# Optimization experiments

Measured on AMD Instinct MI355X. Metric: run time of the kernel, lower is better.

## Reference

```python
import jax, jax.numpy as jnp
import numpy as np

B, S, H, NH, L, V = 1, 2048, 2048, 16, 2, 32000
HD = H // NH            # 128 head dim
ROT = int(HD * 0.25)    # 32 rotary dims
BASE = 10000.0
EPS = 1e-5


def gelu(x):
    # GPT-NeoX tanh-approx gelu (matches the @torch.jit.script gelu)
    val = 0.79788456 * x * (1.0 + 0.044715 * x * x)
    return x * 0.5 * (1.0 + jnp.tanh(val))


def layernorm(x, g, b):
    m = jnp.mean(x, axis=-1, keepdims=True)
    v = jnp.var(x, axis=-1, keepdims=True)
    return (x - m) / jnp.sqrt(v + EPS) * g + b


def rope_cos_sin(seq_len):
    inv_freq = 1.0 / (BASE ** (jnp.arange(0, ROT, 2, dtype=jnp.float32) / ROT))
    t = jnp.arange(seq_len, dtype=jnp.float32)
    freqs = jnp.outer(t, inv_freq)             # [S, ROT/2]
    emb = jnp.concatenate([freqs, freqs], -1)  # [S, ROT]
    return jnp.cos(emb), jnp.sin(emb)


def rotate_half(x):
    half = x.shape[-1] // 2
    return jnp.concatenate([-x[..., half:], x[..., :half]], axis=-1)


def setup_inputs():
    key = jax.random.key(0)
    ks = jax.random.split(key, 8)
    s = 0.02
    return {
        "tokens": jax.random.randint(ks[0], (B, S), 0, V, dtype=jnp.int32),
        "embed": jax.random.normal(ks[1], (V, H), jnp.float32) * s,
        "ln1_g": jnp.ones((L, H), jnp.float32), "ln1_b": jnp.zeros((L, H), jnp.float32),
        "ln2_g": jnp.ones((L, H), jnp.float32), "ln2_b": jnp.zeros((L, H), jnp.float32),
        "qkv_w": jax.random.normal(ks[2], (L, 3 * H, H), jnp.float32) * s,
        "qkv_b": jnp.zeros((L, 3 * H), jnp.float32),
        "attn_out_w": jax.random.normal(ks[3], (L, H, H), jnp.float32) * s,
        "attn_out_b": jnp.zeros((L, H), jnp.float32),
        "fc1_w": jax.random.normal(ks[4], (L, 4 * H, H), jnp.float32) * s,
        "fc1_b": jnp.zeros((L, 4 * H), jnp.float32),
        "fc2_w": jax.random.normal(ks[5], (L, H, 4 * H), jnp.float32) * s,
        "fc2_b": jnp.zeros((L, H), jnp.float32),
        "lnf_g": jnp.ones((H,), jnp.float32), "lnf_b": jnp.zeros((H,), jnp.float32),
        "logits_w": jax.random.normal(ks[6], (V, H), jnp.float32) * s,
    }


def _attn_block(x, qw, qb, ow, ob, cos, sin, mask):
    b, s, _ = x.shape
    qkv = (x @ qw.T + qb).reshape(b, s, NH, 3 * HD)
    q, k, v = qkv[..., :HD], qkv[..., HD:2 * HD], qkv[..., 2 * HD:]
    c = cos[None, :, None, :]
    sn = sin[None, :, None, :]
    q = jnp.concatenate([q[..., :ROT] * c + rotate_half(q[..., :ROT]) * sn, q[..., ROT:]], -1)
    k = jnp.concatenate([k[..., :ROT] * c + rotate_half(k[..., :ROT]) * sn, k[..., ROT:]], -1)
    scores = jnp.einsum('bqhd,bkhd->bhqk', q, k) / jnp.float32(np.sqrt(HD))
    scores = jnp.where(mask, scores, jnp.float32(-10000.0))  # masked_fill -10000
    probs = jax.nn.softmax(scores, axis=-1)
    ctx = jnp.einsum('bhqk,bkhd->bqhd', probs, v).reshape(b, s, H)
    return ctx @ ow.T + ob


def reference(tokens, embed, ln1_g, ln1_b, ln2_g, ln2_b, qkv_w, qkv_b,
              attn_out_w, attn_out_b, fc1_w, fc1_b, fc2_w, fc2_b,
              lnf_g, lnf_b, logits_w):
    seq = tokens.shape[1]
    mask = jnp.tril(jnp.ones((1, 1, seq, seq), dtype=bool))
    cos, sin = rope_cos_sin(seq)
    h = embed[tokens]  # [B,S,H]
    for i in range(L):
        attn = _attn_block(layernorm(h, ln1_g[i], ln1_b[i]),
                           qkv_w[i], qkv_b[i], attn_out_w[i], attn_out_b[i],
                           cos, sin, mask)
        mlp_in = layernorm(h, ln2_g[i], ln2_b[i])
        mlp = gelu(mlp_in @ fc1_w[i].T + fc1_b[i]) @ fc2_w[i].T + fc2_b[i]
        h = h + mlp + attn  # parallel residual
    h = layernorm(h, lnf_g, lnf_b)
    logits = h @ logits_w.T
    return logits
```

## Files before the change

### kernel.cpp

```cpp
#include <hip/hip_runtime.h>
#include <cstdint>
#include <cstddef>

#define S_ 2048
#define H_ 2048
#define NH_ 16
#define HD_ 128
#define L_ 2
#define V_ 32000
#define ROT_ 32

typedef __bf16 bf16x8 __attribute__((ext_vector_type(8)));
typedef float f32x4 __attribute__((ext_vector_type(4)));

__device__ __forceinline__ unsigned short f2bf(float f) {
    unsigned u = __builtin_bit_cast(unsigned, f);
    unsigned r = u + 0x7fffu + ((u >> 16) & 1u);
    return (unsigned short)(r >> 16);
}
__device__ __forceinline__ float bf2f(unsigned short h) {
    return __builtin_bit_cast(float, (unsigned)h << 16);
}
__device__ __forceinline__ float gelu_f(float x) {
    float t = 0.79788456f * x * (1.0f + 0.044715f * x * x);
    return x * 0.5f * (1.0f + tanhf(t));
}

__global__ __launch_bounds__(256) void k_embed(const int* __restrict__ tok,
                                               const float* __restrict__ emb,
                                               float* __restrict__ h) {
    int s = blockIdx.x;
    int t = tok[s];
    const float4* src = (const float4*)(emb + (size_t)t * H_);
    float4* dst = (float4*)(h + (size_t)s * H_);
    for (int i = threadIdx.x; i < H_ / 4; i += 256) dst[i] = src[i];
}

__global__ __launch_bounds__(256) void k_ln(const float* __restrict__ x,
                                            const float* __restrict__ g,
                                            const float* __restrict__ b,
                                            unsigned short* __restrict__ out) {
    int s = blockIdx.x;
    int tid = threadIdx.x;
    const float4* xr = (const float4*)(x + (size_t)s * H_);
    float4 v0 = xr[tid], v1 = xr[tid + 256];
    float s1 = v0.x + v0.y + v0.z + v0.w + v1.x + v1.y + v1.z + v1.w;
    float s2 = v0.x * v0.x + v0.y * v0.y + v0.z * v0.z + v0.w * v0.w +
               v1.x * v1.x + v1.y * v1.y + v1.z * v1.z + v1.w * v1.w;
    #pragma unroll
    for (int off = 32; off > 0; off >>= 1) {
        s1 += __shfl_down(s1, off);
        s2 += __shfl_down(s2, off);
    }
    __shared__ float red[2][4];
    int wave = tid >> 6, lane = tid & 63;
    if (lane == 0) { red[0][wave] = s1; red[1][wave] = s2; }
    __syncthreads();
    s1 = red[0][0] + red[0][1] + red[0][2] + red[0][3];
    s2 = red[1][0] + red[1][1] + red[1][2] + red[1][3];
    float mean = s1 * (1.0f / H_);
    float var = s2 * (1.0f / H_) - mean * mean;
    float rstd = rsqrtf(var + 1e-5f);
    unsigned short* orow = out + (size_t)s * H_;
    int e0 = tid * 4, e1 = (tid + 256) * 4;
    unsigned short h0 = f2bf((v0.x - mean) * rstd * g[e0 + 0] + b[e0 + 0]);
    unsigned short h1 = f2bf((v0.y - mean) * rstd * g[e0 + 1] + b[e0 + 1]);
    unsigned short h2 = f2bf((v0.z - mean) * rstd * g[e0 + 2] + b[e0 + 2]);
    unsigned short h3 = f2bf((v0.w - mean) * rstd * g[e0 + 3] + b[e0 + 3]);
    uint2 p0; p0.x = h0 | ((unsigned)h1 << 16); p0.y = h2 | ((unsigned)h3 << 16);
    ((uint2*)orow)[tid] = p0;
    h0 = f2bf((v1.x - mean) * rstd * g[e1 + 0] + b[e1 + 0]);
    h1 = f2bf((v1.y - mean) * rstd * g[e1 + 1] + b[e1 + 1]);
    h2 = f2bf((v1.z - mean) * rstd * g[e1 + 2] + b[e1 + 2]);
    h3 = f2bf((v1.w - mean) * rstd * g[e1 + 3] + b[e1 + 3]);
    uint2 p1; p1.x = h0 | ((unsigned)h1 << 16); p1.y = h2 | ((unsigned)h3 << 16);
    ((uint2*)orow)[tid + 256] = p1;
}

template <bool BF16OUT, bool GELU, bool BIAS>
__global__ __launch_bounds__(256) void k_gemm(const unsigned short* __restrict__ A,
                                              const float* __restrict__ W,
                                              const float* __restrict__ bias,
                                              void* __restrict__ Cptr,
                                              int M, int N, int K) {
    __shared__ __align__(16) unsigned short sA[128][32];
    __shared__ __align__(16) unsigned short sW[128][32];
    int m0 = blockIdx.y * 128, n0 = blockIdx.x * 128;
    int tid = threadIdx.x, lane = tid & 63, wave = tid >> 6;
    int wm = (wave >> 1) * 64, wn = (wave & 1) * 64;
    int lrow = lane & 15, lq = lane >> 4;
    f32x4 acc[4][4] = {};
    int nk = K >> 5;
    for (int kt = 0; kt < nk; ++kt) {
        int k0 = kt << 5;
        #pragma unroll
        for (int i = 0; i < 2; ++i) {
            int c = tid + i * 256;
            int row = c >> 2, seg = c & 3;
            *(uint4*)&sA[row][seg * 8] =
                *(const uint4*)(A + (size_t)(m0 + row) * K + k0 + seg * 8);
        }
        #pragma unroll
        for (int j = 0; j < 4; ++j) {
            int c = tid + j * 256;
            int row = c >> 3, seg = c & 7;
            float4 v = *(const float4*)(W + (size_t)(n0 + row) * K + k0 + seg * 4);
            unsigned short h0 = f2bf(v.x), h1 = f2bf(v.y), h2 = f2bf(v.z), h3 = f2bf(v.w);
            uint2 p; p.x = h0 | ((unsigned)h1 << 16); p.y = h2 | ((unsigned)h3 << 16);
            *(uint2*)&sW[row][seg * 4] = p;
        }
        __syncthreads();
        bf16x8 af[4], bfr[4];
        #pragma unroll
        for (int i = 0; i < 4; ++i) af[i] = *(const bf16x8*)&sA[wm + i * 16 + lrow][lq * 8];
        #pragma unroll
        for (int j = 0; j < 4; ++j) bfr[j] = *(const bf16x8*)&sW[wn + j * 16 + lrow][lq * 8];
        #pragma unroll
        for (int i = 0; i < 4; ++i)
            #pragma unroll
            for (int j = 0; j < 4; ++j)
                acc[i][j] = __builtin_amdgcn_mfma_f32_16x16x32_bf16(af[i], bfr[j], acc[i][j], 0, 0, 0);
        __syncthreads();
    }
    #pragma unroll
    for (int i = 0; i < 4; ++i) {
        #pragma unroll
        for (int j = 0; j < 4; ++j) {
            int col = n0 + wn + j * 16 + lrow;
            float bb = BIAS ? bias[col] : 0.0f;
            #pragma unroll
            for (int r = 0; r < 4; ++r) {
                int row = m0 + wm + i * 16 + lq * 4 + r;
                float v = acc[i][j][r] + bb;
                if (GELU) v = gelu_f(v);
                if (BF16OUT)
                    ((unsigned short*)Cptr)[(size_t)row * N + col] = f2bf(v);
                else
                    ((float*)Cptr)[(size_t)row * N + col] = v;
            }
        }
    }
}

__global__ __launch_bounds__(256) void k_rope(const unsigned short* __restrict__ qkv,
                                              unsigned short* __restrict__ Qb,
                                              unsigned short* __restrict__ Kb,
                                              unsigned short* __restrict__ Vb) {
    int s = blockIdx.x;
    const unsigned short* row = qkv + (size_t)s * (3 * H_);
    for (int e = threadIdx.x; e < H_; e += 256) {
        int h = e >> 7, d = e & 127;
        int base = h * 384;
        float q = bf2f(row[base + d]);
        float k = bf2f(row[base + 128 + d]);
        float v = bf2f(row[base + 256 + d]);
        if (d < ROT_) {
            int i = d & 15;
            float invf = powf(10000.0f, -(float)i * (1.0f / 16.0f));
            float ang = (float)s * invf;
            float c, sn;
            sincosf(ang, &sn, &c);
            float qo = (d < 16) ? -bf2f(row[base + d + 16]) : bf2f(row[base + d - 16]);
            float ko = (d < 16) ? -bf2f(row[base + 128 + d + 16]) : bf2f(row[base + 128 + d - 16]);
            q = q * c + qo * sn;
            k = k * c + ko * sn;
        }
        size_t o = ((size_t)h * S_ + s) * HD_ + d;
        Qb[o] = f2bf(q);
        Kb[o] = f2bf(k);
        Vb[o] = f2bf(v);
    }
}

#define ATP 24
__global__ __launch_bounds__(256) void k_attn(const unsigned short* __restrict__ Q,
                                              const unsigned short* __restrict__ K,
                                              const unsigned short* __restrict__ V,
                                              unsigned short* __restrict__ ctx) {
    __shared__ __align__(16) unsigned short sQ[64][128 + ATP];
    __shared__ __align__(16) unsigned short sK[64][128 + ATP];
    __shared__ __align__(16) unsigned short sVt[128][64 + ATP];
    __shared__ __align__(16) unsigned short sP[64][64 + ATP];
    int qt = blockIdx.x, h = blockIdx.y;
    int q0 = qt * 64;
    int tid = threadIdx.x, lane = tid & 63, w = tid >> 6;
    int lrow = lane & 15, lq = lane >> 4;
    const unsigned short* Qh = Q + (size_t)h * S_ * HD_;
    const unsigned short* Kh = K + (size_t)h * S_ * HD_;
    const unsigned short* Vh = V + (size_t)h * S_ * HD_;
    for (int c = tid; c < 64 * 16; c += 256) {
        int row = c >> 4, cc = c & 15;
        *(uint4*)&sQ[row][cc * 8] = *(const uint4*)(Qh + (size_t)(q0 + row) * HD_ + cc * 8);
    }
    __syncthreads();
    bf16x8 qf[4];
    #pragma unroll
    for (int kk = 0; kk < 4; ++kk) qf[kk] = *(const bf16x8*)&sQ[w * 16 + lrow][kk * 32 + lq * 8];
    f32x4 o[8] = {};
    float m_i[4], l_i[4];
    #pragma unroll
    for (int r = 0; r < 4; ++r) { m_i[r] = -1e30f; l_i[r] = 0.0f; }
    const float scale = 0.08838834764831845f;
    int ntiles = qt + 1;
    for (int t = 0; t < ntiles; ++t) {
        int k0 = t * 64;
        for (int c = tid; c < 64 * 16; c += 256) {
            int row = c >> 4, cc = c & 15;
            *(uint4*)&sK[row][cc * 8] = *(const uint4*)(Kh + (size_t)(k0 + row) * HD_ + cc * 8);
        }
        for (int c = tid; c < 64 * 32; c += 256) {
            int kv = c >> 5, d0 = (c & 31) * 4;
            ushort4 vv = *(const ushort4*)(Vh + (size_t)(k0 + kv) * HD_ + d0);
            sVt[d0 + 0][kv] = vv.x;
            sVt[d0 + 1][kv] = vv.y;
            sVt[d0 + 2][kv] = vv.z;
            sVt[d0 + 3][kv] = vv.w;
        }
        __syncthreads();
        f32x4 sc[4] = {};
        #pragma unroll
        for (int kk = 0; kk < 4; ++kk) {
            #pragma unroll
            for (int j = 0; j < 4; ++j) {
                bf16x8 kfr = *(const bf16x8*)&sK[j * 16 + lrow][kk * 32 + lq * 8];
                sc[j] = __builtin_amdgcn_mfma_f32_16x16x32_bf16(qf[kk], kfr, sc[j], 0, 0, 0);
            }
        }
        float rmax[4];
        #pragma unroll
        for (int r = 0; r < 4; ++r) {
            int qg = q0 + w * 16 + lq * 4 + r;
            float mx = -1e30f;
            #pragma unroll
            for (int j = 0; j < 4; ++j) {
                int kg = k0 + j * 16 + lrow;
                float vv = sc[j][r] * scale;
                if (kg > qg) vv = -1e30f;
                sc[j][r] = vv;
                mx = fmaxf(mx, vv);
            }
            rmax[r] = mx;
        }
        #pragma unroll
        for (int off = 1; off < 16; off <<= 1)
            #pragma unroll
            for (int r = 0; r < 4; ++r) rmax[r] = fmaxf(rmax[r], __shfl_xor(rmax[r], off, 16));
        float alpha[4];
        #pragma unroll
        for (int r = 0; r < 4; ++r) {
            float mn = fmaxf(m_i[r], rmax[r]);
            alpha[r] = __expf(m_i[r] - mn);
            m_i[r] = mn;
        }
        float rsum[4] = {0.f, 0.f, 0.f, 0.f};
        #pragma unroll
        for (int j = 0; j < 4; ++j)
            #pragma unroll
            for (int r = 0; r < 4; ++r) {
                float p = __expf(sc[j][r] - m_i[r]);
                sc[j][r] = p;
                rsum[r] += p;
            }
        #pragma unroll
        for (int off = 1; off < 16; off <<= 1)
            #pragma unroll
            for (int r = 0; r < 4; ++r) rsum[r] += __shfl_xor(rsum[r], off, 16);
        #pragma unroll
        for (int r = 0; r < 4; ++r) l_i[r] = l_i[r] * alpha[r] + rsum[r];
        #pragma unroll
        for (int j = 0; j < 4; ++j)
            #pragma unroll
            for (int r = 0; r < 4; ++r)
                sP[w * 16 + lq * 4 + r][j * 16 + lrow] = f2bf(sc[j][r]);
        #pragma unroll
        for (int n = 0; n < 8; ++n)
            #pragma unroll
            for (int r = 0; r < 4; ++r) o[n][r] *= alpha[r];
        __syncthreads();
        bf16x8 pa[2];
        #pragma unroll
        for (int kk = 0; kk < 2; ++kk) pa[kk] = *(const bf16x8*)&sP[w * 16 + lrow][kk * 32 + lq * 8];
        #pragma unroll
        for (int n = 0; n < 8; ++n) {
            #pragma unroll
            for (int kk = 0; kk < 2; ++kk) {
                bf16x8 vf = *(const bf16x8*)&sVt[n * 16 + lrow][kk * 32 + lq * 8];
                o[n] = __builtin_amdgcn_mfma_f32_16x16x32_bf16(pa[kk], vf, o[n], 0, 0, 0);
            }
        }
        __syncthreads();
    }
    #pragma unroll
    for (int n = 0; n < 8; ++n)
        #pragma unroll
        for (int r = 0; r < 4; ++r) {
            int row = q0 + w * 16 + lq * 4 + r;
            int d = n * 16 + lrow;
            ctx[(size_t)row * H_ + h * HD_ + d] = f2bf(o[n][r] / l_i[r]);
        }
}

__global__ __launch_bounds__(256) void k_resid(float* __restrict__ h,
                                               const float* __restrict__ a,
                                               const float* __restrict__ m, int n4) {
    int i = blockIdx.x * 256 + threadIdx.x;
    if (i < n4) {
        float4 hv = ((float4*)h)[i];
        float4 av = ((const float4*)a)[i];
        float4 mv = ((const float4*)m)[i];
        hv.x += av.x + mv.x;
        hv.y += av.y + mv.y;
        hv.z += av.z + mv.z;
        hv.w += av.w + mv.w;
        ((float4*)h)[i] = hv;
    }
}

extern "C" void kernel_launch(void* const* d_in, const int* in_sizes, int n_in,
                              void* d_out, int out_size, void* d_ws, size_t ws_size,
                              hipStream_t stream) {
    const int* tokens = (const int*)d_in[0];
    const float* embed = (const float*)d_in[1];
    const float* ln1_g = (const float*)d_in[2];
    const float* ln1_b = (const float*)d_in[3];
    const float* ln2_g = (const float*)d_in[4];
    const float* ln2_b = (const float*)d_in[5];
    const float* qkv_w = (const float*)d_in[6];
    const float* qkv_b = (const float*)d_in[7];
    const float* aow = (const float*)d_in[8];
    const float* aob = (const float*)d_in[9];
    const float* fc1w = (const float*)d_in[10];
    const float* fc1b = (const float*)d_in[11];
    const float* fc2w = (const float*)d_in[12];
    const float* fc2b = (const float*)d_in[13];
    const float* lnfg = (const float*)d_in[14];
    const float* lnfb = (const float*)d_in[15];
    const float* logw = (const float*)d_in[16];

    char* p = (char*)d_ws;
    auto alloc = [&](size_t bytes) {
        char* r = p;
        p += (bytes + 255) & ~(size_t)255;
        return r;
    };
    float* h = (float*)alloc((size_t)S_ * H_ * 4);
    unsigned short* xb = (unsigned short*)alloc((size_t)S_ * H_ * 2);
    unsigned short* qkv = (unsigned short*)alloc((size_t)S_ * 3 * H_ * 2);
    unsigned short* Qb = (unsigned short*)alloc((size_t)NH_ * S_ * HD_ * 2);
    unsigned short* Kb = (unsigned short*)alloc((size_t)NH_ * S_ * HD_ * 2);
    unsigned short* Vb = (unsigned short*)alloc((size_t)NH_ * S_ * HD_ * 2);
    unsigned short* ctx = (unsigned short*)alloc((size_t)S_ * H_ * 2);
    float* attn = (float*)alloc((size_t)S_ * H_ * 4);
    unsigned short* f1 = (unsigned short*)alloc((size_t)S_ * 4 * H_ * 2);
    float* mlp = (float*)alloc((size_t)S_ * H_ * 4);

    k_embed<<<S_, 256, 0, stream>>>(tokens, embed, h);
    for (int l = 0; l < L_; ++l) {
        k_ln<<<S_, 256, 0, stream>>>(h, ln1_g + l * H_, ln1_b + l * H_, xb);
        k_gemm<true, false, true><<<dim3(3 * H_ / 128, S_ / 128), 256, 0, stream>>>(
            xb, qkv_w + (size_t)l * 3 * H_ * H_, qkv_b + l * 3 * H_, qkv, S_, 3 * H_, H_);
        k_rope<<<S_, 256, 0, stream>>>(qkv, Qb, Kb, Vb);
        k_attn<<<dim3(S_ / 64, NH_), 256, 0, stream>>>(Qb, Kb, Vb, ctx);
        k_gemm<false, false, true><<<dim3(H_ / 128, S_ / 128), 256, 0, stream>>>(
            ctx, aow + (size_t)l * H_ * H_, aob + l * H_, attn, S_, H_, H_);
        k_ln<<<S_, 256, 0, stream>>>(h, ln2_g + l * H_, ln2_b + l * H_, xb);
        k_gemm<true, true, true><<<dim3(4 * H_ / 128, S_ / 128), 256, 0, stream>>>(
            xb, fc1w + (size_t)l * 4 * H_ * H_, fc1b + l * 4 * H_, f1, S_, 4 * H_, H_);
        k_gemm<false, false, true><<<dim3(H_ / 128, S_ / 128), 256, 0, stream>>>(
            f1, fc2w + (size_t)l * H_ * 4 * H_, fc2b + l * H_, mlp, S_, H_, 4 * H_);
        k_resid<<<(S_ * H_ / 4 + 255) / 256, 256, 0, stream>>>(h, attn, mlp, S_ * H_ / 4);
    }
    k_ln<<<S_, 256, 0, stream>>>(h, lnfg, lnfb, xb);
    k_gemm<false, false, false><<<dim3(V_ / 128, S_ / 128), 256, 0, stream>>>(
        xb, logw, nullptr, (float*)d_out, S_, V_, H_);
}
```

Measured before the change: 3.020 ms.

## Pre-convert weights to bf16 once and load GEMM tiles directly into LDS

Adds a conversion pass that turns every fp32 weight matrix into bf16 in workspace at the start of each call. The GEMMs then read half-size weights and fill both A and W shared-memory tiles with global_load_lds direct-to-LDS loads, which removes the per-tile fp32-to-bf16 conversion and the register round trip. Since each GEMM reuses a weight tile across 16 M-blocks, the one-time conversion pass is meant to cost less than the repeated converted loads it replaces. It needs extra workspace and falls back to the old path if the workspace is too small.

```diff
diff --git a/kernel.cpp b/kernel.cpp
--- a/kernel.cpp
+++ b/kernel.cpp
@@ -34,6 +34,18 @@
     const float4* src = (const float4*)(emb + (size_t)t * H_);
     float4* dst = (float4*)(h + (size_t)s * H_);
     for (int i = threadIdx.x; i < H_ / 4; i += 256) dst[i] = src[i];
+}
+
+__global__ __launch_bounds__(256) void k_cvt(const float* __restrict__ src,
+                                             unsigned short* __restrict__ dst, int n4) {
+    int stride = gridDim.x * 256;
+    for (int i = blockIdx.x * 256 + threadIdx.x; i < n4; i += stride) {
+        float4 v = ((const float4*)src)[i];
+        uint2 p;
+        p.x = f2bf(v.x) | ((unsigned)f2bf(v.y) << 16);
+        p.y = f2bf(v.z) | ((unsigned)f2bf(v.w) << 16);
+        ((uint2*)dst)[i] = p;
+    }
 }
 
 __global__ __launch_bounds__(256) void k_ln(const float* __restrict__ x,
@@ -77,44 +89,60 @@
     ((uint2*)orow)[tid + 256] = p1;
 }
 
-template <bool BF16OUT, bool GELU, bool BIAS>
+template <bool WB, bool BF16OUT, bool GELU, bool BIAS>
 __global__ __launch_bounds__(256) void k_gemm(const unsigned short* __restrict__ A,
-                                              const float* __restrict__ W,
+                                              const void* __restrict__ Wv,
                                               const float* __restrict__ bias,
                                               void* __restrict__ Cptr,
                                               int M, int N, int K) {
-    __shared__ __align__(16) unsigned short sA[128][32];
-    __shared__ __align__(16) unsigned short sW[128][32];
+    __shared__ __align__(16) unsigned short sA[128 * 32];
+    __shared__ __align__(16) unsigned short sW[128 * 32];
     int m0 = blockIdx.y * 128, n0 = blockIdx.x * 128;
     int tid = threadIdx.x, lane = tid & 63, wave = tid >> 6;
     int wm = (wave >> 1) * 64, wn = (wave & 1) * 64;
     int lrow = lane & 15, lq = lane >> 4;
     f32x4 acc[4][4] = {};
     int nk = K >> 5;
+    const unsigned short* Wb = (const unsigned short*)Wv;
+    const float* Wf = (const float*)Wv;
     for (int kt = 0; kt < nk; ++kt) {
         int k0 = kt << 5;
         #pragma unroll
         for (int i = 0; i < 2; ++i) {
             int c = tid + i * 256;
             int row = c >> 2, seg = c & 3;
-            *(uint4*)&sA[row][seg * 8] =
-                *(const uint4*)(A + (size_t)(m0 + row) * K + k0 + seg * 8);
-        }
-        #pragma unroll
-        for (int j = 0; j < 4; ++j) {
-            int c = tid + j * 256;
-            int row = c >> 3, seg = c & 7;
-            float4 v = *(const float4*)(W + (size_t)(n0 + row) * K + k0 + seg * 4);
-            unsigned short h0 = f2bf(v.x), h1 = f2bf(v.y), h2 = f2bf(v.z), h3 = f2bf(v.w);
-            uint2 p; p.x = h0 | ((unsigned)h1 << 16); p.y = h2 | ((unsigned)h3 << 16);
-            *(uint2*)&sW[row][seg * 4] = p;
+            __builtin_amdgcn_global_load_lds(
+                (const __attribute__((address_space(1))) void*)(A + (size_t)(m0 + row) * K + k0 + seg * 8),
+                (__attribute__((address_space(3))) void*)(sA + (wave * 64 + i * 256) * 8),
+                16, 0, 0);
+        }
+        if constexpr (WB) {
+            #pragma unroll
+            for (int i = 0; i < 2; ++i) {
+                int c = tid + i * 256;
+                int row = c >> 2, seg = c & 3;
+                __builtin_amdgcn_global_load_lds(
+                    (const __attribute__((address_space(1))) void*)(Wb + (size_t)(n0 + row) * K + k0 + seg * 8),
+                    (__attribute__((address_space(3))) void*)(sW + (wave * 64 + i * 256) * 8),
+                    16, 0, 0);
+            }
+        } else {
+            #pragma unroll
+            for (int j = 0; j < 4; ++j) {
+                int c = tid + j * 256;
+                int row = c >> 3, seg = c & 7;
+                float4 v = *(const float4*)(Wf + (size_t)(n0 + row) * K + k0 + seg * 4);
+                unsigned short h0 = f2bf(v.x), h1 = f2bf(v.y), h2 = f2bf(v.z), h3 = f2bf(v.w);
+                uint2 pq; pq.x = h0 | ((unsigned)h1 << 16); pq.y = h2 | ((unsigned)h3 << 16);
+                *(uint2*)&sW[row * 32 + seg * 4] = pq;
+            }
         }
         __syncthreads();
         bf16x8 af[4], bfr[4];
         #pragma unroll
-        for (int i = 0; i < 4; ++i) af[i] = *(const bf16x8*)&sA[wm + i * 16 + lrow][lq * 8];
-        #pragma unroll
-        for (int j = 0; j < 4; ++j) bfr[j] = *(const bf16x8*)&sW[wn + j * 16 + lrow][lq * 8];
+        for (int i = 0; i < 4; ++i) af[i] = *(const bf16x8*)&sA[(wm + i * 16 + lrow) * 32 + lq * 8];
+        #pragma unroll
+        for (int j = 0; j < 4; ++j) bfr[j] = *(const bf16x8*)&sW[(wn + j * 16 + lrow) * 32 + lq * 8];
         #pragma unroll
         for (int i = 0; i < 4; ++i)
             #pragma unroll
@@ -353,24 +381,57 @@
     float* attn = (float*)alloc((size_t)S_ * H_ * 4);
     unsigned short* f1 = (unsigned short*)alloc((size_t)S_ * 4 * H_ * 2);
     float* mlp = (float*)alloc((size_t)S_ * H_ * 4);
+    unsigned short* wqkv = (unsigned short*)alloc((size_t)L_ * 3 * H_ * H_ * 2);
+    unsigned short* waow = (unsigned short*)alloc((size_t)L_ * H_ * H_ * 2);
+    unsigned short* wfc1 = (unsigned short*)alloc((size_t)L_ * 4 * H_ * H_ * 2);
+    unsigned short* wfc2 = (unsigned short*)alloc((size_t)L_ * H_ * 4 * H_ * 2);
+    unsigned short* wlog = (unsigned short*)alloc((size_t)V_ * H_ * 2);
+    bool pre = ((size_t)(p - (char*)d_ws) <= ws_size);
 
     k_embed<<<S_, 256, 0, stream>>>(tokens, embed, h);
+    if (pre) {
+        k_cvt<<<2048, 256, 0, stream>>>(qkv_w, wqkv, L_ * 3 * H_ * H_ / 4);
+        k_cvt<<<2048, 256, 0, stream>>>(aow, waow, L_ * H_ * H_ / 4);
+        k_cvt<<<2048, 256, 0, stream>>>(fc1w, wfc1, L_ * 4 * H_ * H_ / 4);
+        k_cvt<<<2048, 256, 0, stream>>>(fc2w, wfc2, L_ * H_ * 4 * H_ / 4);
+        k_cvt<<<2048, 256, 0, stream>>>(logw, wlog, V_ * H_ / 4);
+    }
     for (int l = 0; l < L_; ++l) {
         k_ln<<<S_, 256, 0, stream>>>(h, ln1_g + l * H_, ln1_b + l * H_, xb);
-        k_gemm<true, false, true><<<dim3(3 * H_ / 128, S_ / 128), 256, 0, stream>>>(
-            xb, qkv_w + (size_t)l * 3 * H_ * H_, qkv_b + l * 3 * H_, qkv, S_, 3 * H_, H_);
+        if (pre)
+            k_gemm<true, true, false, true><<<dim3(3 * H_ / 128, S_ / 128), 256, 0, stream>>>(
+                xb, wqkv + (size_t)l * 3 * H_ * H_, qkv_b + l * 3 * H_, qkv, S_, 3 * H_, H_);
+        else
+            k_gemm<false, true, false, true><<<dim3(3 * H_ / 128, S_ / 128), 256, 0, stream>>>(
+                xb, qkv_w + (size_t)l * 3 * H_ * H_, qkv_b + l * 3 * H_, qkv, S_, 3 * H_, H_);
         k_rope<<<S_, 256, 0, stream>>>(qkv, Qb, Kb, Vb);
         k_attn<<<dim3(S_ / 64, NH_), 256, 0, stream>>>(Qb, Kb, Vb, ctx);
-        k_gemm<false, false, true><<<dim3(H_ / 128, S_ / 128), 256, 0, stream>>>(
-            ctx, aow + (size_t)l * H_ * H_, aob + l * H_, attn, S_, H_, H_);
+        if (pre)
+            k_gemm<true, false, false, true><<<dim3(H_ / 128, S_ / 128), 256, 0, stream>>>(
+                ctx, waow + (size_t)l * H_ * H_, aob + l * H_, attn, S_, H_, H_);
+        else
+            k_gemm<false, false, false, true><<<dim3(H_ / 128, S_ / 128), 256, 0, stream>>>(
+                ctx, aow + (size_t)l * H_ * H_, aob + l * H_, attn, S_, H_, H_);
         k_ln<<<S_, 256, 0, stream>>>(h, ln2_g + l * H_, ln2_b + l * H_, xb);
-        k_gemm<true, true, true><<<dim3(4 * H_ / 128, S_ / 128), 256, 0, stream>>>(
-            xb, fc1w + (size_t)l * 4 * H_ * H_, fc1b + l * 4 * H_, f1, S_, 4 * H_, H_);
-        k_gemm<false, false, true><<<dim3(H_ / 128, S_ / 128), 256, 0, stream>>>(
-            f1, fc2w + (size_t)l * H_ * 4 * H_, fc2b + l * H_, mlp, S_, H_, 4 * H_);
+        if (pre)
+            k_gemm<true, true, true, true><<<dim3(4 * H_ / 128, S_ / 128), 256, 0, stream>>>(
+                xb, wfc1 + (size_t)l * 4 * H_ * H_, fc1b + l * 4 * H_, f1, S_, 4 * H_, H_);
+        else
+            k_gemm<false, true, true, true><<<dim3(4 * H_ / 128, S_ / 128), 256, 0, stream>>>(
+                xb, fc1w + (size_t)l * 4 * H_ * H_, fc1b + l * 4 * H_, f1, S_, 4 * H_, H_);
+        if (pre)
+            k_gemm<true, false, false, true><<<dim3(H_ / 128, S_ / 128), 256, 0, stream>>>(
+                f1, wfc2 + (size_t)l * H_ * 4 * H_, fc2b + l * H_, mlp, S_, H_, 4 * H_);
+        else
+            k_gemm<false, false, false, true><<<dim3(H_ / 128, S_ / 128), 256, 0, stream>>>(
+                f1, fc2w + (size_t)l * H_ * 4 * H_, fc2b + l * H_, mlp, S_, H_, 4 * H_);
         k_resid<<<(S_ * H_ / 4 + 255) / 256, 256, 0, stream>>>(h, attn, mlp, S_ * H_ / 4);
     }
     k_ln<<<S_, 256, 0, stream>>>(h, lnfg, lnfb, xb);
-    k_gemm<false, false, false><<<dim3(V_ / 128, S_ / 128), 256, 0, stream>>>(
-        xb, logw, nullptr, (float*)d_out, S_, V_, H_);
-}
+    if (pre)
+        k_gemm<true, false, false, false><<<dim3(V_ / 128, S_ / 128), 256, 0, stream>>>(
+            xb, wlog, nullptr, (float*)d_out, S_, V_, H_);
+    else
+        k_gemm<false, false, false, false><<<dim3(V_ / 128, S_ / 128), 256, 0, stream>>>(
+            xb, logw, nullptr, (float*)d_out, S_, V_, H_);
+}
```

Measured after the change: 2.634 ms. 1.15x faster.
